# Performance work log

Measured on AMD Instinct MI355X. Metric: run time of the kernel, lower is better.

The kernel has to match this reference:

```python
import jax, jax.numpy as jnp
import numpy as np

M = 5            # Anderson history size
LAM = 1e-4       # Tikhonov regularization on the Gram matrix
MAX_ITER = 50
TOL = 1e-5
BETA = 1.0
ALPHA = 0.9      # damping


def anderson(f, x0, m=M, lam=LAM, max_iter=MAX_ITER, tol=TOL, beta=BETA):
    """Anderson acceleration for fixed-point iteration (faithful to torch ref).

    x0: [bsz, L]. Variable history size n=min(k,m) is handled by masking the
    (m+1)x(m+1) system: inactive slots get an identity row -> alpha_j = 0.
    """
    bsz, L = x0.shape
    dt = x0.dtype
    F0 = f(x0)
    F1 = f(F0)
    X = jnp.zeros((bsz, m, L), dt).at[:, 0].set(x0).at[:, 1].set(F0)
    Fh = jnp.zeros((bsz, m, L), dt).at[:, 0].set(F0).at[:, 1].set(F1)
    eye_m = jnp.eye(m, dtype=dt)

    def body(carry):
        k, X, Fh, _ = carry
        n = jnp.minimum(k, m)
        active = (jnp.arange(m) < n).astype(dt)          # [m]
        G = Fh - X                                        # inactive rows are zero
        Hc = jnp.einsum('bil,bjl->bij', G, G) + lam * eye_m
        m2 = active[:, None] * active[None, :]
        # zero out inactive rows/cols, put 1 on their diagonal (=> alpha_j = 0)
        Hc = Hc * m2 + eye_m * (1.0 - active)
        H = jnp.zeros((bsz, m + 1, m + 1), dt)
        H = H.at[:, 0, 1:].set(active).at[:, 1:, 0].set(active).at[:, 1:, 1:].set(Hc)
        y = jnp.zeros((bsz, m + 1, 1), dt).at[:, 0, 0].set(1.0)
        alpha_c = jnp.linalg.solve(H, y)[:, 1:, 0]        # [bsz, m]
        xnew = beta * jnp.einsum('bm,bml->bl', alpha_c, Fh) \
             + (1.0 - beta) * jnp.einsum('bm,bml->bl', alpha_c, X)
        slot = k % m
        X = X.at[:, slot].set(xnew)
        fnew = f(xnew)
        Fh = Fh.at[:, slot].set(fnew)
        res = jnp.linalg.norm(fnew - xnew) / (1e-5 + jnp.linalg.norm(fnew))
        return (k + 1, X, Fh, res)

    def cond(carry):
        k, _, _, res = carry
        return jnp.logical_and(k < max_iter, res >= tol)

    k, X, Fh, res = jax.lax.while_loop(
        cond, body, (jnp.array(2), X, Fh, jnp.array(np.inf, dt)))
    return X[:, (k - 1) % m]


def make_f(x, maskf, W, b, alpha):
    """Damped forward step: z -> softmax_ch((1-a)z + a*Conv(mask-inject(z)))."""
    bsz, C, H, Wd = x.shape

    def f(zflat):
        z = zflat.reshape(bsz, C, H, Wd)
        zm = z * (1.0 - maskf) + maskf * x               # inject observed parts
        lin = jax.lax.conv_general_dilated(
            zm, W, window_strides=(1, 1), padding='SAME',
            dimension_numbers=('NCHW', 'OIHW', 'NCHW')) + b[None, :, None, None]
        pre = (1.0 - alpha) * z + alpha * lin
        return jax.nn.softmax(pre, axis=1).reshape(bsz, -1)

    return f


def setup_inputs() -> dict:
    key = jax.random.key(0)
    k1, k2, k3 = jax.random.split(key, 3)
    bsz, C, H, Wd = 32, 128, 32, 32
    x = jax.random.normal(k1, (bsz, C, H, Wd), jnp.float32)
    mask = jax.random.randint(k2, (bsz, 1, H, Wd), 0, 2).astype(jnp.int32)
    W = jax.random.normal(k3, (C, C, 3, 3), jnp.float32) * 0.05  # keep map contractive
    b = jnp.zeros((C,), jnp.float32)
    return {"x": x, "W": W, "b": b, "mask": mask}


def reference(x, W, b, mask):
    bsz, C, H, Wd = x.shape
    maskf = mask.astype(x.dtype)
    f = make_f(x, maskf, W, b, ALPHA)
    # z_start = softmax(zeros) over channel dim -> uniform 1/C
    z0 = jnp.full((bsz, C * H * Wd), 1.0 / C, x.dtype)
    zstar = anderson(f, z0)
    zn = f(zstar)            # one extra step, as in the torch forward
    return zn                # [bsz, C*H*W]
```

## Files before the change

kernel.cpp:

```cpp
#include <hip/hip_runtime.h>


typedef unsigned short u16;
using short8 = __attribute__((ext_vector_type(8))) short;
using f32x4  = __attribute__((ext_vector_type(4))) float;

#define SLOT 4194304

struct Ctrl { int done; int last_slot; };

__device__ __forceinline__ u16 f2bf(float f) {
  unsigned u = __builtin_bit_cast(unsigned, f);
  unsigned r = (u + 0x7FFFu + ((u >> 16) & 1u)) >> 16;
  return (u16)r;
}
__device__ __forceinline__ float bf2f(u16 h) {
  unsigned u = ((unsigned)h) << 16;
  return __builtin_bit_cast(float, u);
}

__global__ void __launch_bounds__(256) k_prepw(const float* __restrict__ W,
    u16* __restrict__ Wb, Ctrl* ctrl) {
  if (blockIdx.x == 0 && threadIdx.x == 0) { ctrl->done = 0; ctrl->last_slot = 4; }
  int t = blockIdx.x * 256 + threadIdx.x;
  int o = t >> 14;
  int rem = t & 16383;
  int cout = rem >> 7, cin = rem & 127;
  float v = W[(size_t)cout * 1152 + (size_t)cin * 9 + o];
  Wb[(size_t)o * 16384 + (size_t)cout * 128 + cin] = f2bf(v);
}

__global__ void __launch_bounds__(256) k_prepx(const float* __restrict__ x,
    u16* __restrict__ xsw) {
  int t = blockIdx.x * 256 + threadIdx.x;
  int g = t >> 15, p = t & 32767;
  int nb = p >> 10, gp = p & 1023, px = p & 31;
  short8 xv;
#pragma unroll
  for (int u = 0; u < 8; ++u) {
    float v = x[(size_t)nb * 131072 + (size_t)(g * 8 + u) * 1024 + gp];
    xv[u] = (short)f2bf(v);
  }
  *(short8*)(xsw + (size_t)p * 128 + (size_t)((g ^ (px & 7)) << 3)) = xv;
}

__global__ void __launch_bounds__(256)
__attribute__((amdgpu_waves_per_eu(4, 4)))
k_iter(
    const int e,
    const u16* __restrict__ xsw, const int* __restrict__ mask_,
    const u16* __restrict__ Wb, const float* __restrict__ bias,
    float* __restrict__ Fhp, u16* __restrict__ FhH, u16* __restrict__ Gp,
    float* __restrict__ gram, float* __restrict__ gpart,
    float* __restrict__ resp, Ctrl* __restrict__ ctrl)
{
  __shared__ char smem[27776];
  char*  As       = smem;
  float* rowmax_s = (float*)(smem + 26112);
  float* rowsum_s = (float*)(smem + 26624);
  float* red      = (float*)(smem + 27136);
  float* alpha_s  = (float*)(smem + 27264);
  float* res_s    = (float*)(smem + 27284);
  int*   mk3      = (int*)(smem + 27392);

  if (ctrl->done) return;

  const int tid = threadIdx.x;
  const int wv = tid >> 6, lane = tid & 63;
  const int lhi = lane >> 4, llo = lane & 15;
  const int bhw = blockIdx.x;
  const int lbid = ((bhw & 7) << 7) + (bhw >> 3);
  const int n = lbid >> 5, y0 = lbid & 31;
  const int gpix0 = (n << 10) + (y0 << 5);
  const int slot = e % 5;
  const int nact = e < 5 ? e : 5;
  const size_t base = ((size_t)lbid * 256 + tid) * 16;

  if (e >= 3) {
    if (tid < 64) {
      float sd = 0.f, sf = 0.f;
      for (int i = tid; i < 1024; i += 64) { sd += resp[2 * i]; sf += resp[2 * i + 1]; }
#pragma unroll
      for (int off = 1; off < 64; off <<= 1) { sd += __shfl_xor(sd, off); sf += __shfl_xor(sf, off); }
      if (tid == 0) res_s[0] = sqrtf(sd) / (1e-5f + sqrtf(sf));
    }
    __syncthreads();
    if (res_s[0] < 1e-5f) {
      if (tid == 0) { ctrl->done = 1; ctrl->last_slot = (e - 1) % 5; }
      return;
    }
  }

  if (tid < 96) {
    int r = tid >> 5, xx = tid & 31;
    int gy = y0 - 1 + r;
    mk3[tid] = ((unsigned)gy < 32u) ? mask_[(n << 10) + (gy << 5) + xx] : 0;
  }
  if (e >= 1 && tid >= 96 && tid < 101) {
    int j = tid - 96;
    float s = 0.f;
#pragma unroll
    for (int c = 0; c < 32; ++c) s += gpart[(size_t)((n << 5) + c) * 5 + j];
    int sp = (e - 1) % 5;
    gram[n * 25 + sp * 5 + j] = s;
    gram[n * 25 + j * 5 + sp] = s;
  }
  __syncthreads();
  if (e >= 2) {
    if (tid == 0) {
      float A[6][7];
      for (int i = 0; i < 5; ++i)
        for (int j = 0; j < 5; ++j)
          A[i + 1][j + 1] = (i < nact && j < nact)
              ? gram[n * 25 + i * 5 + j] + ((i == j) ? 1e-4f : 0.f)
              : ((i == j) ? 1.f : 0.f);
      A[0][0] = 0.f;
      for (int j = 0; j < 5; ++j) { float aj = (j < nact) ? 1.f : 0.f; A[0][j + 1] = aj; A[j + 1][0] = aj; }
      A[0][6] = 1.f;
      for (int i = 1; i < 6; ++i) A[i][6] = 0.f;
      for (int c = 0; c < 6; ++c) {
        int p = c; float mx = fabsf(A[c][c]);
        for (int r = c + 1; r < 6; ++r) { float v = fabsf(A[r][c]); if (v > mx) { mx = v; p = r; } }
        if (p != c) for (int q = c; q < 7; ++q) { float tmp = A[c][q]; A[c][q] = A[p][q]; A[p][q] = tmp; }
        float piv = A[c][c];
        for (int r = c + 1; r < 6; ++r) {
          float fr = A[r][c] / piv;
          for (int q = c; q < 7; ++q) A[r][q] -= fr * A[c][q];
        }
      }
      float sol[6];
      for (int r = 5; r >= 0; --r) {
        float s = A[r][6];
        for (int q = r + 1; q < 6; ++q) s -= A[r][q] * sol[q];
        sol[r] = s / A[r][r];
      }
      for (int j = 0; j < 5; ++j) alpha_s[j] = sol[j + 1];
    }
  } else if (tid < 5) {
    alpha_s[tid] = (tid == 0) ? 1.f : 0.f;
  }
  __syncthreads();

  float a0 = 1.f, a1 = 0.f, a2 = 0.f, a3 = 0.f, a4 = 0.f;
  if (e >= 1) { a0 = alpha_s[0]; a1 = alpha_s[1]; a2 = alpha_s[2]; a3 = alpha_s[3]; a4 = alpha_s[4]; }

#pragma unroll
  for (int uu = 0; uu < 4; ++uu) {
    int u = (uu << 8) + tid;
    int row3 = u >> 9;
    int gy = y0 - 1 + (row3 << 1);
    int idx = u & 511;
    int px = idx >> 4, grp = idx & 15;
    char* dst = As + (row3 << 1) * 8704 + ((px + 1) << 8) + ((grp ^ (px & 7)) << 4);
    short8 w = {0, 0, 0, 0, 0, 0, 0, 0};
    if ((unsigned)gy < 32u) {
      int gpix = (n << 10) + (gy << 5) + px;
      size_t off = (size_t)gpix * 128 + (size_t)((grp ^ (px & 7)) << 3);
      if (mk3[(row3 << 6) + px]) {
        w = *(const short8*)(xsw + off);
      } else if (e == 0) {
#pragma unroll
        for (int i = 0; i < 8; ++i) w[i] = (short)0x3C00;
      } else {
        short8 h0, h1, h2, h3, h4;
        h0 = *(const short8*)(FhH + off);
        if (nact > 1) h1 = *(const short8*)(FhH + SLOT + off);
        if (nact > 2) h2 = *(const short8*)(FhH + 2 * (size_t)SLOT + off);
        if (nact > 3) h3 = *(const short8*)(FhH + 3 * (size_t)SLOT + off);
        if (nact > 4) h4 = *(const short8*)(FhH + 4 * (size_t)SLOT + off);
        f32x4 va, vb;
#pragma unroll
        for (int i = 0; i < 4; ++i) { va[i] = a0 * bf2f((u16)h0[i]); vb[i] = a0 * bf2f((u16)h0[4 + i]); }
        if (nact > 1) {
#pragma unroll
          for (int i = 0; i < 4; ++i) { va[i] += a1 * bf2f((u16)h1[i]); vb[i] += a1 * bf2f((u16)h1[4 + i]); }
        }
        if (nact > 2) {
#pragma unroll
          for (int i = 0; i < 4; ++i) { va[i] += a2 * bf2f((u16)h2[i]); vb[i] += a2 * bf2f((u16)h2[4 + i]); }
        }
        if (nact > 3) {
#pragma unroll
          for (int i = 0; i < 4; ++i) { va[i] += a3 * bf2f((u16)h3[i]); vb[i] += a3 * bf2f((u16)h3[4 + i]); }
        }
        if (nact > 4) {
#pragma unroll
          for (int i = 0; i < 4; ++i) { va[i] += a4 * bf2f((u16)h4[i]); vb[i] += a4 * bf2f((u16)h4[4 + i]); }
        }
#pragma unroll
        for (int i = 0; i < 4; ++i) { w[i] = (short)f2bf(va[i]); w[4 + i] = (short)f2bf(vb[i]); }
      }
    }
    *(short8*)dst = w;
  }

  f32x4 zv[4];
  if (e == 0) {
    const f32x4 cz = {0.0078125f, 0.0078125f, 0.0078125f, 0.0078125f};
    zv[0] = cz; zv[1] = cz; zv[2] = cz; zv[3] = cz;
  } else {
    const float* fb = Fhp + base;
    f32x4 t0[4], t1[4], t2[4], t3[4], t4[4];
#pragma unroll
    for (int q = 0; q < 4; ++q) t0[q] = *(const f32x4*)(fb + q * 4);
    if (nact > 1) {
#pragma unroll
      for (int q = 0; q < 4; ++q) t1[q] = *(const f32x4*)(fb + SLOT + q * 4);
    }
    if (nact > 2) {
#pragma unroll
      for (int q = 0; q < 4; ++q) t2[q] = *(const f32x4*)(fb + 2 * SLOT + q * 4);
    }
    if (nact > 3) {
#pragma unroll
      for (int q = 0; q < 4; ++q) t3[q] = *(const f32x4*)(fb + 3 * SLOT + q * 4);
    }
    if (nact > 4) {
#pragma unroll
      for (int q = 0; q < 4; ++q) t4[q] = *(const f32x4*)(fb + 4 * SLOT + q * 4);
    }
#pragma unroll
    for (int q = 0; q < 4; ++q) zv[q] = a0 * t0[q];
    if (nact > 1) {
#pragma unroll
      for (int q = 0; q < 4; ++q) zv[q] += a1 * t1[q];
    }
    if (nact > 2) {
#pragma unroll
      for (int q = 0; q < 4; ++q) zv[q] += a2 * t2[q];
    }
    if (nact > 3) {
#pragma unroll
      for (int q = 0; q < 4; ++q) zv[q] += a3 * t3[q];
    }
    if (nact > 4) {
#pragma unroll
      for (int q = 0; q < 4; ++q) zv[q] += a4 * t4[q];
    }
  }

#pragma unroll
  for (int m2 = 0; m2 < 2; ++m2)
#pragma unroll
    for (int nf = 0; nf < 2; ++nf)
#pragma unroll
      for (int rr = 0; rr < 4; ++rr) {
        int p = (m2 << 4) + (lhi << 2) + rr;
        int ch = (wv << 5) + (nf << 4) + llo;
        int sg = (ch >> 3) ^ (p & 7);
        u16 w;
        if (mk3[32 + p])
          w = xsw[(size_t)(gpix0 + p) * 128 + (sg << 3) + (ch & 7)];
        else
          w = f2bf(zv[(m2 << 1) + nf][rr]);
        *(u16*)(As + 8704 + ((p + 1) << 8) + (sg << 4) + ((ch & 7) << 1)) = w;
      }

  if (tid < 96) {
    int r = tid >> 5, cc = tid & 31;
    int col = (cc < 16) ? 0 : 33, gc = cc & 15;
    f32x4 zz = {0.f, 0.f, 0.f, 0.f};
    *(f32x4*)(As + r * 8704 + (col << 8) + (gc << 4)) = zz;
  }
  __syncthreads();

  f32x4 acc[2][2];
  {
    const f32x4 z4 = {0.f, 0.f, 0.f, 0.f};
    acc[0][0] = z4; acc[0][1] = z4; acc[1][0] = z4; acc[1][1] = z4;
  }
#pragma unroll
  for (int o = 0; o < 9; ++o) {
    const int dy = o / 3, dx = o % 3;
    short8 bfr[2][4];
#pragma unroll
    for (int nf = 0; nf < 2; ++nf)
#pragma unroll
      for (int kk = 0; kk < 4; ++kk) {
        int ch = (wv << 5) + (nf << 4) + llo;
        bfr[nf][kk] = *(const short8*)(Wb + o * 16384 + ch * 128 + ((kk << 2) + lhi) * 8);
      }
#pragma unroll
    for (int kk = 0; kk < 4; ++kk) {
      const int kg = (kk << 2) + lhi;
#pragma unroll
      for (int m2 = 0; m2 < 2; ++m2) {
        int p = (m2 << 4) + llo;
        int cl = p + dx;
        int sg = kg ^ ((cl - 1) & 7);
        short8 af = *(const short8*)(As + dy * 8704 + (cl << 8) + (sg << 4));
#pragma unroll
        for (int nf = 0; nf < 2; ++nf)
          acc[m2][nf] = __builtin_amdgcn_mfma_f32_16x16x32_bf16(af, bfr[nf][kk], acc[m2][nf], 0, 0, 0);
      }
    }
  }

  const float bc0 = bias[(wv << 5) + llo];
  const float bc1 = bias[(wv << 5) + 16 + llo];
#pragma unroll
  for (int m2 = 0; m2 < 2; ++m2)
#pragma unroll
    for (int rr = 0; rr < 4; ++rr) {
      acc[m2][0][rr] = 0.1f * zv[m2 << 1][rr] + 0.9f * (acc[m2][0][rr] + bc0);
      acc[m2][1][rr] = 0.1f * zv[(m2 << 1) + 1][rr] + 0.9f * (acc[m2][1][rr] + bc1);
    }
#pragma unroll
  for (int m2 = 0; m2 < 2; ++m2)
#pragma unroll
    for (int rr = 0; rr < 4; ++rr) {
      float v = fmaxf(acc[m2][0][rr], acc[m2][1][rr]);
      v = fmaxf(v, __shfl_xor(v, 1)); v = fmaxf(v, __shfl_xor(v, 2));
      v = fmaxf(v, __shfl_xor(v, 4)); v = fmaxf(v, __shfl_xor(v, 8));
      if (llo == 0) rowmax_s[(((m2 << 4) + (lhi << 2) + rr) << 2) + wv] = v;
    }
  __syncthreads();
#pragma unroll
  for (int m2 = 0; m2 < 2; ++m2)
#pragma unroll
    for (int rr = 0; rr < 4; ++rr) {
      int p = (m2 << 4) + (lhi << 2) + rr;
      f32x4 m0 = *(const f32x4*)&rowmax_s[p << 2];
      float M = fmaxf(fmaxf(m0[0], m0[1]), fmaxf(m0[2], m0[3]));
      float e0 = __expf(acc[m2][0][rr] - M);
      float e1 = __expf(acc[m2][1][rr] - M);
      acc[m2][0][rr] = e0; acc[m2][1][rr] = e1;
      float s = e0 + e1;
      s += __shfl_xor(s, 1); s += __shfl_xor(s, 2);
      s += __shfl_xor(s, 4); s += __shfl_xor(s, 8);
      if (llo == 0) rowsum_s[(p << 2) + wv] = s;
    }
  __syncthreads();

  float sd = 0.f, sf = 0.f;
#pragma unroll
  for (int m2 = 0; m2 < 2; ++m2) {
    f32x4 fr0, fr1;
#pragma unroll
    for (int rr = 0; rr < 4; ++rr) {
      int p = (m2 << 4) + (lhi << 2) + rr;
      f32x4 s0 = *(const f32x4*)&rowsum_s[p << 2];
      float S = s0[0] + s0[1] + s0[2] + s0[3];
      float invS = 1.0f / S;
      float f0 = acc[m2][0][rr] * invS;
      float f1 = acc[m2][1][rr] * invS;
      acc[m2][0][rr] = f0; acc[m2][1][rr] = f1;
      fr0[rr] = f0; fr1[rr] = f1;
      float g0 = f0 - zv[m2 << 1][rr];
      float g1 = f1 - zv[(m2 << 1) + 1][rr];
      sd += g0 * g0 + g1 * g1; sf += f0 * f0 + f1 * f1;
      int ch0 = (wv << 5) + llo, ch1 = ch0 + 16;
      size_t rb = (size_t)slot * SLOT + (size_t)(gpix0 + p) * 128;
      FhH[rb + ((((ch0 >> 3) ^ (p & 7)) << 3) | (ch0 & 7))] = f2bf(f0);
      FhH[rb + ((((ch1 >> 3) ^ (p & 7)) << 3) | (ch1 & 7))] = f2bf(f1);
    }
    *(f32x4*)(Fhp + (size_t)slot * SLOT + base + (m2 << 3)) = fr0;
    *(f32x4*)(Fhp + (size_t)slot * SLOT + base + (m2 << 3) + 4) = fr1;
  }
  {
    short8 h0, h1;
#pragma unroll
    for (int m2 = 0; m2 < 2; ++m2)
#pragma unroll
      for (int nf = 0; nf < 2; ++nf)
#pragma unroll
        for (int rr = 0; rr < 4; ++rr) {
          int q = (((m2 << 1) + nf) << 2) + rr;
          u16 gb16 = f2bf(acc[m2][nf][rr] - zv[(m2 << 1) + nf][rr]);
          if (q < 8) h0[q] = (short)gb16; else h1[q - 8] = (short)gb16;
        }
    u16* Gs = Gp + (size_t)slot * SLOT + base;
    *(short8*)(Gs) = h0;
    *(short8*)(Gs + 8) = h1;
    const int jmax = e < 4 ? e : 4;
    short8 qa[5], qb[5];
#pragma unroll
    for (int j = 0; j < 5; ++j) {
      if (j != slot && j <= jmax) {
        qa[j] = *(const short8*)(Gp + (size_t)j * SLOT + base);
        qb[j] = *(const short8*)(Gp + (size_t)j * SLOT + base + 8);
      }
    }
    float gacc[5];
#pragma unroll
    for (int j = 0; j < 5; ++j) {
      if (j > jmax) { gacc[j] = 0.f; continue; }
      if (j == slot) {
        float a = 0.f;
#pragma unroll
        for (int m2 = 0; m2 < 2; ++m2)
#pragma unroll
          for (int nf = 0; nf < 2; ++nf)
#pragma unroll
            for (int rr = 0; rr < 4; ++rr) {
              float gd = acc[m2][nf][rr] - zv[(m2 << 1) + nf][rr];
              a += gd * gd;
            }
        gacc[j] = a;
      } else {
        float a = 0.f;
#pragma unroll
        for (int m2 = 0; m2 < 2; ++m2)
#pragma unroll
          for (int nf = 0; nf < 2; ++nf)
#pragma unroll
            for (int rr = 0; rr < 4; ++rr) {
              int q = (((m2 << 1) + nf) << 2) + rr;
              float gd = acc[m2][nf][rr] - zv[(m2 << 1) + nf][rr];
              float hv = bf2f((u16)(q < 8 ? qa[j][q] : qb[j][q - 8]));
              a += gd * hv;
            }
        gacc[j] = a;
      }
    }
    float vals[7] = {gacc[0], gacc[1], gacc[2], gacc[3], gacc[4], sd, sf};
#pragma unroll
    for (int i = 0; i < 7; ++i) {
      float v = vals[i];
#pragma unroll
      for (int off = 1; off < 64; off <<= 1) v += __shfl_xor(v, off);
      if (lane == 0) red[(wv << 3) + i] = v;
    }
  }
  __syncthreads();
  if (tid < 7) {
    float s = 0.f;
#pragma unroll
    for (int w = 0; w < 4; ++w) s += red[(w << 3) + tid];
    if (tid < 5)       gpart[(size_t)lbid * 5 + tid] = s;
    else if (tid == 5) resp[lbid * 2] = s;
    else               resp[lbid * 2 + 1] = s;
  }
}

__global__ void __launch_bounds__(256) k_out(const float* __restrict__ Fhp,
    const Ctrl* __restrict__ ctrl, float* __restrict__ out)
{
  __shared__ float T[32 * 132];
  int slot = ctrl->last_slot;
  const int tid = threadIdx.x;
  const int wv = tid >> 6, lane = tid & 63;
  const int lhi = lane >> 4, llo = lane & 15;
  const int lbid = blockIdx.x;
  const int n = lbid >> 5, y0 = lbid & 31;
  const size_t base = (size_t)slot * SLOT + ((size_t)lbid * 256 + tid) * 16;
#pragma unroll
  for (int m2 = 0; m2 < 2; ++m2)
#pragma unroll
    for (int nf = 0; nf < 2; ++nf) {
      f32x4 v = *(const f32x4*)(Fhp + base + (((m2 << 1) + nf) << 2));
#pragma unroll
      for (int rr = 0; rr < 4; ++rr) {
        int p = (m2 << 4) + (lhi << 2) + rr;
        int ch = (wv << 5) + (nf << 4) + llo;
        T[p * 132 + ch] = v[rr];
      }
    }
  __syncthreads();
  int c = tid >> 1, h = tid & 1;
  float* ob = out + (((size_t)(n << 7) + c) << 10) + (y0 << 5) + (h << 4);
#pragma unroll
  for (int i2 = 0; i2 < 4; ++i2) {
    f32x4 v;
#pragma unroll
    for (int i = 0; i < 4; ++i) v[i] = T[((h << 4) + (i2 << 2) + i) * 132 + c];
    *(f32x4*)(ob + (i2 << 2)) = v;
  }
}

extern "C" void kernel_launch(void* const* d_in, const int* in_sizes, int n_in,
                              void* d_out, int out_size, void* d_ws, size_t ws_size,
                              hipStream_t stream) {
  const float* x    = (const float*)d_in[0];
  const float* W    = (const float*)d_in[1];
  const float* bias = (const float*)d_in[2];
  const int*   mask = (const int*)d_in[3];
  float* out = (float*)d_out;
  char* ws = (char*)d_ws;

  float* Fhp   = (float*)(ws + 0);
  u16*   FhH   = (u16*)(ws + 83886080);
  u16*   Gp    = (u16*)(ws + 125829120);
  u16*   xsw   = (u16*)(ws + 167772160);
  u16*   Wb    = (u16*)(ws + 176160768);
  float* gram  = (float*)(ws + 176455680);
  float* gpart = (float*)(ws + 176458880);
  float* resp  = (float*)(ws + 176479360);
  Ctrl*  ctrl  = (Ctrl*)(ws + 176487552);

  k_prepw<<<576, 256, 0, stream>>>(W, Wb, ctrl);
  k_prepx<<<2048, 256, 0, stream>>>(x, xsw);
  for (int e = 0; e < 50; ++e)
    k_iter<<<1024, 256, 0, stream>>>(e, xsw, mask, Wb, bias,
                                     Fhp, FhH, Gp, gram, gpart, resp, ctrl);
  k_out<<<1024, 256, 0, stream>>>(Fhp, ctrl, out);
  (void)in_sizes; (void)n_in; (void)out_size; (void)ws_size;
}
```

Measured before the change: 422.3 us.

## Split work across eight waves per block with one channel fragment each

Doubles the block size of the iteration and output kernels from 256 to 512 threads. Each wave now owns 16 output channels instead of 32, which halves the per-thread accumulators, weight fragments and history registers. The cross-wave softmax and reduction buffers grow from four to eight waves. The aim is to raise latency hiding through more waves per CU, at the cost of more cross-wave shared-memory reductions and more threads sharing the same staging loads.

Result: slower. 501.8 us (+18.8%).

```diff
diff --git a/kernel.cpp b/kernel.cpp
--- a/kernel.cpp
+++ b/kernel.cpp
@@ -44,8 +44,8 @@
   *(short8*)(xsw + (size_t)p * 128 + (size_t)((g ^ (px & 7)) << 3)) = xv;
 }
 
-__global__ void __launch_bounds__(256)
-__attribute__((amdgpu_waves_per_eu(4, 4)))
+__global__ void __launch_bounds__(512)
+__attribute__((amdgpu_waves_per_eu(8, 8)))
 k_iter(
     const int e,
     const u16* __restrict__ xsw, const int* __restrict__ mask_,
@@ -54,14 +54,14 @@
     float* __restrict__ gram, float* __restrict__ gpart,
     float* __restrict__ resp, Ctrl* __restrict__ ctrl)
 {
-  __shared__ char smem[27776];
+  __shared__ char smem[28928];
   char*  As       = smem;
   float* rowmax_s = (float*)(smem + 26112);
-  float* rowsum_s = (float*)(smem + 26624);
-  float* red      = (float*)(smem + 27136);
-  float* alpha_s  = (float*)(smem + 27264);
-  float* res_s    = (float*)(smem + 27284);
-  int*   mk3      = (int*)(smem + 27392);
+  float* rowsum_s = (float*)(smem + 27136);
+  float* red      = (float*)(smem + 28160);
+  float* alpha_s  = (float*)(smem + 28416);
+  float* res_s    = (float*)(smem + 28440);
+  int*   mk3      = (int*)(smem + 28544);
 
   if (ctrl->done) return;
 
@@ -72,9 +72,10 @@
   const int lbid = ((bhw & 7) << 7) + (bhw >> 3);
   const int n = lbid >> 5, y0 = lbid & 31;
   const int gpix0 = (n << 10) + (y0 << 5);
+  const int ch = (wv << 4) + llo;
   const int slot = e % 5;
   const int nact = e < 5 ? e : 5;
-  const size_t base = ((size_t)lbid * 256 + tid) * 16;
+  const size_t base = ((size_t)lbid * 512 + tid) * 8;
 
   if (e >= 3) {
     if (tid < 64) {
@@ -145,8 +146,8 @@
   if (e >= 1) { a0 = alpha_s[0]; a1 = alpha_s[1]; a2 = alpha_s[2]; a3 = alpha_s[3]; a4 = alpha_s[4]; }
 
 #pragma unroll
-  for (int uu = 0; uu < 4; ++uu) {
-    int u = (uu << 8) + tid;
+  for (int uu = 0; uu < 2; ++uu) {
+    int u = (uu << 9) + tid;
     int row3 = u >> 9;
     int gy = y0 - 1 + (row3 << 1);
     int idx = u & 511;
@@ -194,67 +195,64 @@
     *(short8*)dst = w;
   }
 
-  f32x4 zv[4];
+  f32x4 zv[2];
   if (e == 0) {
     const f32x4 cz = {0.0078125f, 0.0078125f, 0.0078125f, 0.0078125f};
-    zv[0] = cz; zv[1] = cz; zv[2] = cz; zv[3] = cz;
+    zv[0] = cz; zv[1] = cz;
   } else {
     const float* fb = Fhp + base;
-    f32x4 t0[4], t1[4], t2[4], t3[4], t4[4];
-#pragma unroll
-    for (int q = 0; q < 4; ++q) t0[q] = *(const f32x4*)(fb + q * 4);
+    f32x4 t0[2], t1[2], t2[2], t3[2], t4[2];
+#pragma unroll
+    for (int q = 0; q < 2; ++q) t0[q] = *(const f32x4*)(fb + q * 4);
     if (nact > 1) {
 #pragma unroll
-      for (int q = 0; q < 4; ++q) t1[q] = *(const f32x4*)(fb + SLOT + q * 4);
+      for (int q = 0; q < 2; ++q) t1[q] = *(const f32x4*)(fb + SLOT + q * 4);
     }
     if (nact > 2) {
 #pragma unroll
-      for (int q = 0; q < 4; ++q) t2[q] = *(const f32x4*)(fb + 2 * SLOT + q * 4);
+      for (int q = 0; q < 2; ++q) t2[q] = *(const f32x4*)(fb + 2 * SLOT + q * 4);
     }
     if (nact > 3) {
 #pragma unroll
-      for (int q = 0; q < 4; ++q) t3[q] = *(const f32x4*)(fb + 3 * SLOT + q * 4);
+      for (int q = 0; q < 2; ++q) t3[q] = *(const f32x4*)(fb + 3 * SLOT + q * 4);
     }
     if (nact > 4) {
 #pragma unroll
-      for (int q = 0; q < 4; ++q) t4[q] = *(const f32x4*)(fb + 4 * SLOT + q * 4);
-    }
-#pragma unroll
-    for (int q = 0; q < 4; ++q) zv[q] = a0 * t0[q];
+      for (int q = 0; q < 2; ++q) t4[q] = *(const f32x4*)(fb + 4 * SLOT + q * 4);
+    }
+#pragma unroll
+    for (int q = 0; q < 2; ++q) zv[q] = a0 * t0[q];
     if (nact > 1) {
 #pragma unroll
-      for (int q = 0; q < 4; ++q) zv[q] += a1 * t1[q];
+      for (int q = 0; q < 2; ++q) zv[q] += a1 * t1[q];
     }
     if (nact > 2) {
 #pragma unroll
-      for (int q = 0; q < 4; ++q) zv[q] += a2 * t2[q];
+      for (int q = 0; q < 2; ++q) zv[q] += a2 * t2[q];
     }
     if (nact > 3) {
 #pragma unroll
-      for (int q = 0; q < 4; ++q) zv[q] += a3 * t3[q];
+      for (int q = 0; q < 2; ++q) zv[q] += a3 * t3[q];
     }
     if (nact > 4) {
 #pragma unroll
-      for (int q = 0; q < 4; ++q) zv[q] += a4 * t4[q];
+      for (int q = 0; q < 2; ++q) zv[q] += a4 * t4[q];
     }
   }
 
 #pragma unroll
   for (int m2 = 0; m2 < 2; ++m2)
 #pragma unroll
-    for (int nf = 0; nf < 2; ++nf)
-#pragma unroll
-      for (int rr = 0; rr < 4; ++rr) {
-        int p = (m2 << 4) + (lhi << 2) + rr;
-        int ch = (wv << 5) + (nf << 4) + llo;
-        int sg = (ch >> 3) ^ (p & 7);
-        u16 w;
-        if (mk3[32 + p])
-          w = xsw[(size_t)(gpix0 + p) * 128 + (sg << 3) + (ch & 7)];
-        else
-          w = f2bf(zv[(m2 << 1) + nf][rr]);
-        *(u16*)(As + 8704 + ((p + 1) << 8) + (sg << 4) + ((ch & 7) << 1)) = w;
-      }
+    for (int rr = 0; rr < 4; ++rr) {
+      int p = (m2 << 4) + (lhi << 2) + rr;
+      int sg = (ch >> 3) ^ (p & 7);
+      u16 w;
+      if (mk3[32 + p])
+        w = xsw[(size_t)(gpix0 + p) * 128 + (sg << 3) + (ch & 7)];
+      else
+        w = f2bf(zv[m2][rr]);
+      *(u16*)(As + 8704 + ((p + 1) << 8) + (sg << 4) + ((ch & 7) << 1)) = w;
+    }
 
   if (tid < 96) {
     int r = tid >> 5, cc = tid & 31;
@@ -264,22 +262,18 @@
   }
   __syncthreads();
 
-  f32x4 acc[2][2];
+  f32x4 acc[2];
   {
     const f32x4 z4 = {0.f, 0.f, 0.f, 0.f};
-    acc[0][0] = z4; acc[0][1] = z4; acc[1][0] = z4; acc[1][1] = z4;
+    acc[0] = z4; acc[1] = z4;
   }
 #pragma unroll
   for (int o = 0; o < 9; ++o) {
     const int dy = o / 3, dx = o % 3;
-    short8 bfr[2][4];
-#pragma unroll
-    for (int nf = 0; nf < 2; ++nf)
-#pragma unroll
-      for (int kk = 0; kk < 4; ++kk) {
-        int ch = (wv << 5) + (nf << 4) + llo;
-        bfr[nf][kk] = *(const short8*)(Wb + o * 16384 + ch * 128 + ((kk << 2) + lhi) * 8);
-      }
+    short8 bfr[4];
+#pragma unroll
+    for (int kk = 0; kk < 4; ++kk)
+      bfr[kk] = *(const short8*)(Wb + o * 16384 + ch * 128 + ((kk << 2) + lhi) * 8);
 #pragma unroll
     for (int kk = 0; kk < 4; ++kk) {
       const int kg = (kk << 2) + lhi;
@@ -289,30 +283,25 @@
         int cl = p + dx;
         int sg = kg ^ ((cl - 1) & 7);
         short8 af = *(const short8*)(As + dy * 8704 + (cl << 8) + (sg << 4));
-#pragma unroll
-        for (int nf = 0; nf < 2; ++nf)
-          acc[m2][nf] = __builtin_amdgcn_mfma_f32_16x16x32_bf16(af, bfr[nf][kk], acc[m2][nf], 0, 0, 0);
+        acc[m2] = __builtin_amdgcn_mfma_f32_16x16x32_bf16(af, bfr[kk], acc[m2], 0, 0, 0);
       }
     }
   }
 
-  const float bc0 = bias[(wv << 5) + llo];
-  const float bc1 = bias[(wv << 5) + 16 + llo];
+  const float bc = bias[ch];
 #pragma unroll
   for (int m2 = 0; m2 < 2; ++m2)
 #pragma unroll
+    for (int rr = 0; rr < 4; ++rr)
+      acc[m2][rr] = 0.1f * zv[m2][rr] + 0.9f * (acc[m2][rr] + bc);
+#pragma unroll
+  for (int m2 = 0; m2 < 2; ++m2)
+#pragma unroll
     for (int rr = 0; rr < 4; ++rr) {
-      acc[m2][0][rr] = 0.1f * zv[m2 << 1][rr] + 0.9f * (acc[m2][0][rr] + bc0);
-      acc[m2][1][rr] = 0.1f * zv[(m2 << 1) + 1][rr] + 0.9f * (acc[m2][1][rr] + bc1);
-    }
-#pragma unroll
-  for (int m2 = 0; m2 < 2; ++m2)
-#pragma unroll
-    for (int rr = 0; rr < 4; ++rr) {
-      float v = fmaxf(acc[m2][0][rr], acc[m2][1][rr]);
+      float v = acc[m2][rr];
       v = fmaxf(v, __shfl_xor(v, 1)); v = fmaxf(v, __shfl_xor(v, 2));
       v = fmaxf(v, __shfl_xor(v, 4)); v = fmaxf(v, __shfl_xor(v, 8));
-      if (llo == 0) rowmax_s[(((m2 << 4) + (lhi << 2) + rr) << 2) + wv] = v;
+      if (llo == 0) rowmax_s[(((m2 << 4) + (lhi << 2) + rr) << 3) + wv] = v;
     }
   __syncthreads();
 #pragma unroll
@@ -320,98 +309,77 @@
 #pragma unroll
     for (int rr = 0; rr < 4; ++rr) {
       int p = (m2 << 4) + (lhi << 2) + rr;
-      f32x4 m0 = *(const f32x4*)&rowmax_s[p << 2];
-      float M = fmaxf(fmaxf(m0[0], m0[1]), fmaxf(m0[2], m0[3]));
-      float e0 = __expf(acc[m2][0][rr] - M);
-      float e1 = __expf(acc[m2][1][rr] - M);
-      acc[m2][0][rr] = e0; acc[m2][1][rr] = e1;
-      float s = e0 + e1;
+      f32x4 m0 = *(const f32x4*)&rowmax_s[p << 3];
+      f32x4 m1 = *(const f32x4*)&rowmax_s[(p << 3) + 4];
+      float M = fmaxf(fmaxf(fmaxf(m0[0], m0[1]), fmaxf(m0[2], m0[3])),
+                      fmaxf(fmaxf(m1[0], m1[1]), fmaxf(m1[2], m1[3])));
+      float ev = __expf(acc[m2][rr] - M);
+      acc[m2][rr] = ev;
+      float s = ev;
       s += __shfl_xor(s, 1); s += __shfl_xor(s, 2);
       s += __shfl_xor(s, 4); s += __shfl_xor(s, 8);
-      if (llo == 0) rowsum_s[(p << 2) + wv] = s;
+      if (llo == 0) rowsum_s[(p << 3) + wv] = s;
     }
   __syncthreads();
 
   float sd = 0.f, sf = 0.f;
 #pragma unroll
   for (int m2 = 0; m2 < 2; ++m2) {
-    f32x4 fr0, fr1;
+    f32x4 fr;
 #pragma unroll
     for (int rr = 0; rr < 4; ++rr) {
       int p = (m2 << 4) + (lhi << 2) + rr;
-      f32x4 s0 = *(const f32x4*)&rowsum_s[p << 2];
-      float S = s0[0] + s0[1] + s0[2] + s0[3];
-      float invS = 1.0f / S;
-      float f0 = acc[m2][0][rr] * invS;
-      float f1 = acc[m2][1][rr] * invS;
-      acc[m2][0][rr] = f0; acc[m2][1][rr] = f1;
-      fr0[rr] = f0; fr1[rr] = f1;
-      float g0 = f0 - zv[m2 << 1][rr];
-      float g1 = f1 - zv[(m2 << 1) + 1][rr];
-      sd += g0 * g0 + g1 * g1; sf += f0 * f0 + f1 * f1;
-      int ch0 = (wv << 5) + llo, ch1 = ch0 + 16;
-      size_t rb = (size_t)slot * SLOT + (size_t)(gpix0 + p) * 128;
-      FhH[rb + ((((ch0 >> 3) ^ (p & 7)) << 3) | (ch0 & 7))] = f2bf(f0);
-      FhH[rb + ((((ch1 >> 3) ^ (p & 7)) << 3) | (ch1 & 7))] = f2bf(f1);
-    }
-    *(f32x4*)(Fhp + (size_t)slot * SLOT + base + (m2 << 3)) = fr0;
-    *(f32x4*)(Fhp + (size_t)slot * SLOT + base + (m2 << 3) + 4) = fr1;
+      f32x4 s0 = *(const f32x4*)&rowsum_s[p << 3];
+      f32x4 s1 = *(const f32x4*)&rowsum_s[(p << 3) + 4];
+      float S = s0[0] + s0[1] + s0[2] + s0[3] + s1[0] + s1[1] + s1[2] + s1[3];
+      float fnew = acc[m2][rr] * (1.0f / S);
+      acc[m2][rr] = fnew;
+      fr[rr] = fnew;
+      float gd = fnew - zv[m2][rr];
+      sd += gd * gd; sf += fnew * fnew;
+      int p2 = p & 7;
+      FhH[(size_t)slot * SLOT + (size_t)(gpix0 + p) * 128 +
+          ((((ch >> 3) ^ p2) << 3) | (ch & 7))] = f2bf(fnew);
+    }
+    *(f32x4*)(Fhp + (size_t)slot * SLOT + base + (m2 << 2)) = fr;
   }
   {
-    short8 h0, h1;
+    short8 g8;
 #pragma unroll
     for (int m2 = 0; m2 < 2; ++m2)
 #pragma unroll
-      for (int nf = 0; nf < 2; ++nf)
-#pragma unroll
-        for (int rr = 0; rr < 4; ++rr) {
-          int q = (((m2 << 1) + nf) << 2) + rr;
-          u16 gb16 = f2bf(acc[m2][nf][rr] - zv[(m2 << 1) + nf][rr]);
-          if (q < 8) h0[q] = (short)gb16; else h1[q - 8] = (short)gb16;
-        }
-    u16* Gs = Gp + (size_t)slot * SLOT + base;
-    *(short8*)(Gs) = h0;
-    *(short8*)(Gs + 8) = h1;
+      for (int rr = 0; rr < 4; ++rr)
+        g8[(m2 << 2) + rr] = (short)f2bf(acc[m2][rr] - zv[m2][rr]);
+    *(short8*)(Gp + (size_t)slot * SLOT + base) = g8;
     const int jmax = e < 4 ? e : 4;
-    short8 qa[5], qb[5];
-#pragma unroll
-    for (int j = 0; j < 5; ++j) {
-      if (j != slot && j <= jmax) {
+    short8 qa[5];
+#pragma unroll
+    for (int j = 0; j < 5; ++j)
+      if (j != slot && j <= jmax)
         qa[j] = *(const short8*)(Gp + (size_t)j * SLOT + base);
-        qb[j] = *(const short8*)(Gp + (size_t)j * SLOT + base + 8);
-      }
-    }
     float gacc[5];
 #pragma unroll
     for (int j = 0; j < 5; ++j) {
       if (j > jmax) { gacc[j] = 0.f; continue; }
+      float a = 0.f;
       if (j == slot) {
-        float a = 0.f;
 #pragma unroll
         for (int m2 = 0; m2 < 2; ++m2)
 #pragma unroll
-          for (int nf = 0; nf < 2; ++nf)
-#pragma unroll
-            for (int rr = 0; rr < 4; ++rr) {
-              float gd = acc[m2][nf][rr] - zv[(m2 << 1) + nf][rr];
-              a += gd * gd;
-            }
-        gacc[j] = a;
+          for (int rr = 0; rr < 4; ++rr) {
+            float gd = acc[m2][rr] - zv[m2][rr];
+            a += gd * gd;
+          }
       } else {
-        float a = 0.f;
 #pragma unroll
         for (int m2 = 0; m2 < 2; ++m2)
 #pragma unroll
-          for (int nf = 0; nf < 2; ++nf)
-#pragma unroll
-            for (int rr = 0; rr < 4; ++rr) {
-              int q = (((m2 << 1) + nf) << 2) + rr;
-              float gd = acc[m2][nf][rr] - zv[(m2 << 1) + nf][rr];
-              float hv = bf2f((u16)(q < 8 ? qa[j][q] : qb[j][q - 8]));
-              a += gd * hv;
-            }
-        gacc[j] = a;
+          for (int rr = 0; rr < 4; ++rr) {
+            float gd = acc[m2][rr] - zv[m2][rr];
+            a += gd * bf2f((u16)qa[j][(m2 << 2) + rr]);
+          }
       }
+      gacc[j] = a;
     }
     float vals[7] = {gacc[0], gacc[1], gacc[2], gacc[3], gacc[4], sd, sf};
 #pragma unroll
@@ -426,14 +394,14 @@
   if (tid < 7) {
     float s = 0.f;
 #pragma unroll
-    for (int w = 0; w < 4; ++w) s += red[(w << 3) + tid];
+    for (int w = 0; w < 8; ++w) s += red[(w << 3) + tid];
     if (tid < 5)       gpart[(size_t)lbid * 5 + tid] = s;
     else if (tid == 5) resp[lbid * 2] = s;
     else               resp[lbid * 2 + 1] = s;
   }
 }
 
-__global__ void __launch_bounds__(256) k_out(const float* __restrict__ Fhp,
+__global__ void __launch_bounds__(512) k_out(const float* __restrict__ Fhp,
     const Ctrl* __restrict__ ctrl, float* __restrict__ out)
 {
   __shared__ float T[32 * 132];
@@ -443,29 +411,27 @@
   const int lhi = lane >> 4, llo = lane & 15;
   const int lbid = blockIdx.x;
   const int n = lbid >> 5, y0 = lbid & 31;
-  const size_t base = (size_t)slot * SLOT + ((size_t)lbid * 256 + tid) * 16;
-#pragma unroll
-  for (int m2 = 0; m2 < 2; ++m2)
-#pragma unroll
-    for (int nf = 0; nf < 2; ++nf) {
-      f32x4 v = *(const f32x4*)(Fhp + base + (((m2 << 1) + nf) << 2));
-#pragma unroll
-      for (int rr = 0; rr < 4; ++rr) {
-        int p = (m2 << 4) + (lhi << 2) + rr;
-        int ch = (wv << 5) + (nf << 4) + llo;
-        T[p * 132 + ch] = v[rr];
-      }
-    }
-  __syncthreads();
-  int c = tid >> 1, h = tid & 1;
-  float* ob = out + (((size_t)(n << 7) + c) << 10) + (y0 << 5) + (h << 4);
-#pragma unroll
-  for (int i2 = 0; i2 < 4; ++i2) {
-    f32x4 v;
-#pragma unroll
-    for (int i = 0; i < 4; ++i) v[i] = T[((h << 4) + (i2 << 2) + i) * 132 + c];
-    *(f32x4*)(ob + (i2 << 2)) = v;
-  }
+  const size_t base = (size_t)slot * SLOT + ((size_t)lbid * 512 + tid) * 8;
+#pragma unroll
+  for (int m2 = 0; m2 < 2; ++m2) {
+    f32x4 v = *(const f32x4*)(Fhp + base + (m2 << 2));
+#pragma unroll
+    for (int rr = 0; rr < 4; ++rr) {
+      int p = (m2 << 4) + (lhi << 2) + rr;
+      T[p * 132 + (wv << 4) + llo] = v[rr];
+    }
+  }
+  __syncthreads();
+  int c = tid >> 2, sub = tid & 3;
+  float* ob = out + (((size_t)(n << 7) + c) << 10) + (y0 << 5) + (sub << 3);
+  f32x4 v0, v1;
+#pragma unroll
+  for (int i = 0; i < 4; ++i) {
+    v0[i] = T[((sub << 3) + i) * 132 + c];
+    v1[i] = T[((sub << 3) + 4 + i) * 132 + c];
+  }
+  *(f32x4*)ob = v0;
+  *(f32x4*)(ob + 4) = v1;
 }
 
 extern "C" void kernel_launch(void* const* d_in, const int* in_sizes, int n_in,
@@ -491,8 +457,8 @@
   k_prepw<<<576, 256, 0, stream>>>(W, Wb, ctrl);
   k_prepx<<<2048, 256, 0, stream>>>(x, xsw);
   for (int e = 0; e < 50; ++e)
-    k_iter<<<1024, 256, 0, stream>>>(e, xsw, mask, Wb, bias,
+    k_iter<<<1024, 512, 0, stream>>>(e, xsw, mask, Wb, bias,
                                      Fhp, FhH, Gp, gram, gpart, resp, ctrl);
-  k_out<<<1024, 256, 0, stream>>>(Fhp, ctrl, out);
+  k_out<<<1024, 512, 0, stream>>>(Fhp, ctrl, out);
   (void)in_sizes; (void)n_in; (void)out_size; (void)ws_size;
 }
```
